# Kernel tuning notes

Hardware: AMD Instinct MI355X
Metric: run time of the kernel (lower is better)

Reference implementation:

```python
import jax, jax.numpy as jnp
import numpy as np
import math

H = 12
DH = 64
MAX_POS = 1024

def setup_inputs() -> dict:
    key = jax.random.key(0)
    ks = jax.random.split(key, 8)
    B, L, D = 2, 1024, 768
    s = 0.02
    return {
        "hidden_states": jax.random.normal(ks[0], (B, L, D), jnp.float32),
        "attention_mask": jnp.zeros((B, 1, 1, L), jnp.float32),
        "struct_matrix": jax.random.uniform(ks[1], (5, B, 1, L, L), jnp.float32),
        "Wq": jax.random.normal(ks[2], (D, D), jnp.float32) * s,
        "bq": jnp.zeros((D,), jnp.float32),
        "Wk": jax.random.normal(ks[3], (D, D), jnp.float32) * s,
        "bk": jnp.zeros((D,), jnp.float32),
        "Wv": jax.random.normal(ks[4], (D, D), jnp.float32) * s,
        "bv": jnp.zeros((D,), jnp.float32),
        "dist_emb": jax.random.normal(ks[5], (2 * MAX_POS - 1, DH), jnp.float32) * s,
        "ssan_w": jax.random.normal(ks[6], (5, H, DH, DH), jnp.float32) * s,
        "abs_bias": jnp.zeros((5, H), jnp.float32),
    }

def reference(hidden_states, attention_mask, struct_matrix, Wq, bq, Wk, bk, Wv, bv, dist_emb, ssan_w, abs_bias):
    B, L, D = hidden_states.shape

    def heads(x):  # [B,L,D] -> [B,H,L,dh]
        return x.reshape(B, L, H, DH).transpose(0, 2, 1, 3)

    q = heads(hidden_states @ Wq + bq)
    k = heads(hidden_states @ Wk + bk)
    v = heads(hidden_states @ Wv + bv)

    scores = jnp.einsum('bhqd,bhkd->bhqk', q, k)

    # relative_key_query positional scores
    pos_ids = jnp.arange(L)
    distance = pos_ids[:, None] - pos_ids[None, :]          # [L,L]
    pos = dist_emb[distance + MAX_POS - 1]                  # [L,L,dh]
    scores = scores + jnp.einsum('bhld,lrd->bhlr', q, pos)
    scores = scores + jnp.einsum('bhrd,lrd->bhlr', k, pos)

    scores = scores / math.sqrt(DH)
    scores = scores + attention_mask

    # 5 SSAN bilinear bias terms, masked by structural matrices
    for i in range(5):
        bias = jnp.einsum('bhqd,hde,bhke->bhqk', q, ssan_w[i], k)
        scores = scores + (bias + abs_bias[i][None, :, None, None]) * struct_matrix[i]

    probs = jax.nn.softmax(scores, axis=-1)
    ctx = jnp.einsum('bhqk,bhkd->bqhd', probs, v).reshape(B, L, D)
    return ctx
```

## Files before the change

### kernel.cpp

```cpp
#include <hip/hip_runtime.h>
#include <math.h>

#define NB 2
#define NL 1024
#define ND 768
#define NH 12
#define DH 64

typedef _Float16 f16;
typedef _Float16 f16x2 __attribute__((ext_vector_type(2)));
typedef _Float16 f16x4 __attribute__((ext_vector_type(4)));
typedef _Float16 f16x8 __attribute__((ext_vector_type(8)));
typedef float f32x4 __attribute__((ext_vector_type(4)));

#define MFMA16(a, b, c) __builtin_amdgcn_mfma_f32_16x16x32_f16((a), (b), (c), 0, 0, 0)

__device__ __forceinline__ void soft_barrier() {
    asm volatile("s_waitcnt lgkmcnt(0)\n\ts_barrier" ::: "memory");
}

__global__ __launch_bounds__(256) void prep_kernel(
    const float* __restrict__ hs,
    const float* __restrict__ Wq, const float* __restrict__ Wk,
    const float* __restrict__ Wv, const float* __restrict__ sw,
    const float* __restrict__ de,
    f16* __restrict__ hsf, f16* __restrict__ wt, f16* __restrict__ swt,
    f16* __restrict__ de16)
{
    __shared__ float sT[64 * 66];
    const int t = threadIdx.x;
    const int tile = blockIdx.x;

    if (tile < 768) {
        const int base = tile * 2048 + t * 8;
        float4 a = *(const float4*)&hs[base];
        float4 b = *(const float4*)&hs[base + 4];
        f16x8 hv;
        hv[0] = (f16)a.x; hv[1] = (f16)a.y; hv[2] = (f16)a.z; hv[3] = (f16)a.w;
        hv[4] = (f16)b.x; hv[5] = (f16)b.y; hv[6] = (f16)b.z; hv[7] = (f16)b.w;
        *(f16x8*)&hsf[base] = hv;
        return;
    }
    if (tile >= 1260) {
        const int base = (tile - 1260) * 2048 + t * 8;
        if (base < 2047 * 64) {
            float4 a = *(const float4*)&de[base];
            float4 b = *(const float4*)&de[base + 4];
            f16x8 hv;
            hv[0] = (f16)a.x; hv[1] = (f16)a.y; hv[2] = (f16)a.z; hv[3] = (f16)a.w;
            hv[4] = (f16)b.x; hv[5] = (f16)b.y; hv[6] = (f16)b.z; hv[7] = (f16)b.w;
            *(f16x8*)&de16[base] = hv;
        }
        return;
    }

    const float* S; f16* D; int sRS, dRS;
    const int ti = tile - 768;
    if (ti < 432) {
        const int mat = ti / 144, r2 = ti % 144, ht = r2 / 12, kt = r2 % 12;
        const float* W = (mat == 0) ? Wq : (mat == 1) ? Wk : Wv;
        S = W + (size_t)(kt * 64) * ND + ht * 64;
        D = wt + (size_t)((mat * NH + ht) * 64) * ND + kt * 64;
        sRS = ND; dRS = ND;
    } else {
        const int i = ti - 432;
        S = sw + (size_t)i * 4096;
        D = swt + (size_t)i * 4096;
        sRS = 64; dRS = 64;
    }

    {
        const int kk = t >> 2, nb = (t & 3) * 16;
        float v[16];
        #pragma unroll
        for (int j = 0; j < 4; ++j)
            *(float4*)&v[4 * j] = *(const float4*)&S[(size_t)kk * sRS + nb + 4 * j];
        #pragma unroll
        for (int jj = 0; jj < 16; ++jj)
            sT[(nb + jj) * 66 + kk] = v[jj];
    }
    soft_barrier();
    {
        const int n = t >> 2, kb = (t & 3) * 16;
        f16 tmp[16];
        #pragma unroll
        for (int j = 0; j < 8; ++j) {
            float2 x = *(float2*)&sT[n * 66 + kb + 2 * j];
            tmp[2 * j]     = (f16)x.x;
            tmp[2 * j + 1] = (f16)x.y;
        }
        *(f16x8*)&D[(size_t)n * dRS + kb]     = *(f16x8*)&tmp[0];
        *(f16x8*)&D[(size_t)n * dRS + kb + 8] = *(f16x8*)&tmp[8];
    }
}

__global__ __launch_bounds__(256, 2) void qkv_kernel(
    const f16* __restrict__ hsf, const f16* __restrict__ wt,
    const float* __restrict__ bq, const float* __restrict__ bk,
    const float* __restrict__ bv,
    f16* __restrict__ qf, f16* __restrict__ kf, f16* __restrict__ vt)
{
    __shared__ f16 sAB[2][2][128 * 72];

    const int m0 = blockIdx.x * 128;
    const int n0 = blockIdx.y * 128;
    const int mat = n0 / 768;
    const int h0  = (n0 % 768) / 64;
    const int bb  = m0 >> 10;
    const int l0  = m0 & 1023;

    const int t = threadIdx.x, lane = t & 63, w = t >> 6;
    const int quad = lane >> 4, l15 = lane & 15;
    const int wm = w >> 1, wn = w & 1;

    const float* bias = (mat == 0) ? bq : (mat == 1) ? bk : bv;

    const int srow = t >> 1;
    const int scol = (t & 1) * 32;
    const f16* Ag = hsf + (size_t)(m0 + srow) * ND + scol;
    const f16* Bg = wt  + (size_t)(n0 + srow) * ND + scol;

    f16x8 ar[4], br[4];
    f32x4 acc[4][4];
    #pragma unroll
    for (int mi = 0; mi < 4; ++mi)
        #pragma unroll
        for (int ni = 0; ni < 4; ++ni)
            acc[mi][ni] = (f32x4){0.f, 0.f, 0.f, 0.f};

    #pragma unroll
    for (int j = 0; j < 4; ++j) {
        ar[j] = *(const f16x8*)&Ag[8 * j];
        br[j] = *(const f16x8*)&Bg[8 * j];
    }
    #pragma unroll
    for (int j = 0; j < 4; ++j) {
        *(f16x8*)&sAB[0][0][srow * 72 + scol + 8 * j] = ar[j];
        *(f16x8*)&sAB[0][1][srow * 72 + scol + 8 * j] = br[j];
    }

    for (int kt2 = 0; kt2 < 12; ++kt2) {
        const int cur = kt2 & 1;
        soft_barrier();
        if (kt2 < 11) {
            const int k0 = (kt2 + 1) * 64;
            #pragma unroll
            for (int j = 0; j < 4; ++j) {
                ar[j] = *(const f16x8*)&Ag[k0 + 8 * j];
                br[j] = *(const f16x8*)&Bg[k0 + 8 * j];
            }
        }
        #pragma unroll
        for (int kk = 0; kk < 64; kk += 32) {
            const int ko = kk + quad * 8;
            f16x8 af[4], bf[4];
            #pragma unroll
            for (int i = 0; i < 4; ++i) {
                af[i] = *(f16x8*)&sAB[cur][0][(64 * wm + 16 * i + l15) * 72 + ko];
                bf[i] = *(f16x8*)&sAB[cur][1][(64 * wn + 16 * i + l15) * 72 + ko];
            }
            #pragma unroll
            for (int mi = 0; mi < 4; ++mi)
                #pragma unroll
                for (int ni = 0; ni < 4; ++ni)
                    acc[mi][ni] = MFMA16(af[mi], bf[ni], acc[mi][ni]);
        }
        if (kt2 < 11) {
            #pragma unroll
            for (int j = 0; j < 4; ++j) {
                *(f16x8*)&sAB[cur ^ 1][0][srow * 72 + scol + 8 * j] = ar[j];
                *(f16x8*)&sAB[cur ^ 1][1][srow * 72 + scol + 8 * j] = br[j];
            }
        }
    }
    soft_barrier();

    f16* sC = (f16*)sAB;
    float bz[4];
    #pragma unroll
    for (int ni = 0; ni < 4; ++ni)
        bz[ni] = bias[(n0 % 768) + 64 * wn + 16 * ni + l15];

    #pragma unroll
    for (int mi = 0; mi < 4; ++mi)
        #pragma unroll
        for (int ni = 0; ni < 4; ++ni) {
            const int col = 64 * wn + 16 * ni + l15;
            #pragma unroll
            for (int r = 0; r < 4; ++r) {
                const int row = 64 * wm + 16 * mi + 4 * quad + r;
                const f16 v = (f16)(acc[mi][ni][r] + bz[ni]);
                if (mat == 2) sC[col * 136 + row] = v;
                else          sC[row * 136 + col] = v;
            }
        }
    soft_barrier();

    if (mat < 2) {
        const int row = t >> 1, half = t & 1;
        f16* dst = ((mat == 0) ? qf : kf)
                 + ((size_t)(bb * NH + h0 + half) * NL + l0 + row) * DH;
        #pragma unroll
        for (int j = 0; j < 8; ++j)
            *(f16x8*)&dst[8 * j] = *(f16x8*)&sC[row * 136 + 64 * half + 8 * j];
    } else {
        const int c = t >> 1, half = t & 1;
        const int d = c & 63, hh = h0 + (c >> 6);
        f16* dst = vt + ((size_t)(bb * NH + hh) * DH + d) * NL + l0 + 64 * half;
        #pragma unroll
        for (int j = 0; j < 8; ++j)
            *(f16x8*)&dst[8 * j] = *(f16x8*)&sC[c * 136 + 64 * half + 8 * j];
    }
}

__global__ __launch_bounds__(256, 2) void attn_kernel(
    const f16* __restrict__ qf, const f16* __restrict__ kf,
    const f16* __restrict__ vt, const f16* __restrict__ swt,
    const float* __restrict__ mask, const float* __restrict__ struct_m,
    const f16* __restrict__ de16, const float* __restrict__ abs_bias,
    float* __restrict__ out)
{
    __shared__ f16 sK[64 * 72];
    __shared__ f16 sVt[2][64 * 72];
    __shared__ f16 sE[96 * 72];
    __shared__ f16 sQEl[96 * 34];
    __shared__ f16 sKEl[96 * 34];
    __shared__ float sS[32 * 68];
    __shared__ f16 sP[32 * 72];
    __shared__ float sAlpha[32], sL[32];

    const int l0 = blockIdx.x * 32;
    const int bh = blockIdx.y;
    const int bb = bh / NH, h = bh % NH;
    const int t  = threadIdx.x;
    const int lane  = t & 63;
    const int w     = t >> 6;
    const int quad  = lane >> 4;
    const int l15   = lane & 15;
    const int msub  = w >> 1;
    const int npair = w & 1;

    f16x8 aQ[2], aW[5][2];
    {
        const size_t qrow = ((size_t)bh * NL + l0 + 16 * msub + l15) * DH;
        #pragma unroll
        for (int K = 0; K < 2; ++K)
            aQ[K] = *(const f16x8*)&qf[qrow + 32 * K + 8 * quad];
    }

    {
        #pragma unroll
        for (int b = 0; b < 2; ++b) {
            const int pb0  = (b == 0) ? 0 : 3;
            const int pcnt = (b == 0) ? 3 : 2;
            #pragma unroll
            for (int pi = 0; pi < 3; ++pi) {
                if (pi < pcnt) {
                    const int p = pb0 + pi;
                    const f16* Wp = swt + ((size_t)(p * NH + h)) * 64 * 64;
                    #pragma unroll
                    for (int ntl = 0; ntl < 2; ++ntl) {
                        const int nt = 2 * npair + ntl;
                        f32x4 c = (f32x4){0.f, 0.f, 0.f, 0.f};
                        #pragma unroll
                        for (int K = 0; K < 2; ++K) {
                            f16x8 bw = *(const f16x8*)&Wp[(size_t)(16 * nt + l15) * 64 + 32 * K + 8 * quad];
                            c = MFMA16(aQ[K], bw, c);
                        }
                        #pragma unroll
                        for (int r = 0; r < 4; ++r)
                            sE[(pi * 32 + 16 * msub + 4 * quad + r) * 72 + 16 * nt + l15] = (f16)c[r];
                    }
                }
            }
            soft_barrier();
            #pragma unroll
            for (int pi = 0; pi < 3; ++pi) {
                if (pi < pcnt) {
                    #pragma unroll
                    for (int K = 0; K < 2; ++K)
                        aW[pb0 + pi][K] =
                            *(const f16x8*)&sE[(pi * 32 + 16 * msub + l15) * 72 + 32 * K + 8 * quad];
                }
            }
            soft_barrier();
        }
    }

    float ab[5];
    #pragma unroll
    for (int p = 0; p < 5; ++p) ab[p] = abs_bias[p * NH + h];

    float pf_st[5][2][4], pf_mask[2];
    f16x8 kreg[2], vreg[2], ereg[3];

    auto issue_kv = [&](int r0s) {
        const int row = t >> 3, col = (t & 7) * 8;
        const f16* ks = kf + ((size_t)bh * NL + r0s) * DH;
        kreg[0] = *(const f16x8*)&ks[row * 64 + col];
        kreg[1] = *(const f16x8*)&ks[(row + 32) * 64 + col];
        const f16* vs = vt + (size_t)bh * DH * NL + r0s;
        vreg[0] = *(const f16x8*)&vs[(size_t)row * NL + col];
        vreg[1] = *(const f16x8*)&vs[(size_t)(row + 32) * NL + col];
    };
    auto write_kv = [&](int buf) {
        const int row = t >> 3, col = (t & 7) * 8;
        *(f16x8*)&sK[row * 72 + col]             = kreg[0];
        *(f16x8*)&sK[(row + 32) * 72 + col]      = kreg[1];
        *(f16x8*)&sVt[buf][row * 72 + col]       = vreg[0];
        *(f16x8*)&sVt[buf][(row + 32) * 72 + col] = vreg[1];
    };
    auto issue_E = [&](int r0s) {
        const int ebase = l0 - r0s + 960;
        #pragma unroll
        for (int p2 = 0; p2 < 3; ++p2) {
            const int idx = t + 256 * p2;
            const int er = idx >> 3, colE = (idx & 7) * 8;
            if (er < 95)
                ereg[p2] = *(const f16x8*)&de16[(size_t)(ebase + er) * DH + colE];
        }
    };
    auto write_E = [&]() {
        #pragma unroll
        for (int p2 = 0; p2 < 3; ++p2) {
            const int idx = t + 256 * p2;
            const int er = idx >> 3, colE = (idx & 7) * 8;
            if (er < 95)
                *(f16x8*)&sE[er * 72 + colE] = ereg[p2];
        }
    };
    auto prefetch = [&](int r0s) {
        #pragma unroll
        for (int n = 0; n < 2; ++n) {
            const int j = 32 * npair + 16 * n + l15;
            pf_mask[n] = mask[bb * NL + r0s + j];
            #pragma unroll
            for (int r = 0; r < 4; ++r) {
                const int i = 16 * msub + 4 * quad + r;
                #pragma unroll
                for (int p = 0; p < 5; ++p)
                    pf_st[p][n][r] =
                        struct_m[((size_t)(p * NB + bb) * NL + l0 + i) * NL + r0s + j];
            }
        }
    };

    issue_kv(0);
    issue_E(0);
    write_kv(0);
    write_E();
    prefetch(0);

    const int sm_i = t >> 3;
    const int sm_jb = t & 7;
    float m_cur = -INFINITY, l_cur = 0.f;
    f32x4 O[2];
    O[0] = (f32x4){0.f, 0.f, 0.f, 0.f};
    O[1] = (f32x4){0.f, 0.f, 0.f, 0.f};

    soft_barrier();

    for (int kt = 0; kt < 16; ++kt) {
        const int cur = kt & 1;

        {
            const int krow = (16 * w + l15) * 72;
            f16x8 ak0 = *(f16x8*)&sK[krow + quad * 8];
            f16x8 ak1 = *(f16x8*)&sK[krow + 32 + quad * 8];
            #pragma unroll
            for (int c = 0; c < 3; ++c) {
                const int nt = 3 - w + c;
                const int erow = (16 * nt + l15) * 72;
                f16x8 e0 = *(f16x8*)&sE[erow + quad * 8];
                f16x8 e1 = *(f16x8*)&sE[erow + 32 + quad * 8];
                f32x4 ck = (f32x4){0.f, 0.f, 0.f, 0.f};
                ck = MFMA16(ak0, e0, ck);
                ck = MFMA16(ak1, e1, ck);
                const int base = (16 * nt + l15) * 34 + 16 * w + 4 * quad;
                f16x2 lo = {(f16)ck[0], (f16)ck[1]};
                f16x2 hi = {(f16)ck[2], (f16)ck[3]};
                *(f16x2*)&sKEl[base]     = lo;
                *(f16x2*)&sKEl[base + 2] = hi;
            }
            const int qs = 3 * npair + msub;
            const int qc = 3 - npair;
            #pragma unroll
            for (int c = 0; c < 3; ++c) {
                if (c < qc) {
                    const int nt = qs + c;
                    const int erow = (16 * nt + l15) * 72;
                    f16x8 e0 = *(f16x8*)&sE[erow + quad * 8];
                    f16x8 e1 = *(f16x8*)&sE[erow + 32 + quad * 8];
                    f32x4 cq = (f32x4){0.f, 0.f, 0.f, 0.f};
                    cq = MFMA16(aQ[0], e0, cq);
                    cq = MFMA16(aQ[1], e1, cq);
                    const int base = (16 * nt + l15) * 34 + 16 * msub + 4 * quad;
                    f16x2 lo = {(f16)cq[0], (f16)cq[1]};
                    f16x2 hi = {(f16)cq[2], (f16)cq[3]};
                    *(f16x2*)&sQEl[base]     = lo;
                    *(f16x2*)&sQEl[base + 2] = hi;
                }
            }
        }
        soft_barrier();

        {
            if (kt < 15) {
                issue_kv((kt + 1) * 64);
                issue_E((kt + 1) * 64);
            }

            f32x4 acc[2][6];
            #pragma unroll
            for (int n = 0; n < 2; ++n)
                #pragma unroll
                for (int p = 0; p < 6; ++p)
                    acc[n][p] = (f32x4){0.f, 0.f, 0.f, 0.f};

            #pragma unroll
            for (int K = 0; K < 2; ++K) {
                const int koff = K * 32 + quad * 8;
                f16x8 bk2[2];
                #pragma unroll
                for (int n = 0; n < 2; ++n)
                    bk2[n] = *(f16x8*)&sK[(32 * npair + 16 * n + l15) * 72 + koff];
                #pragma unroll
                for (int n = 0; n < 2; ++n)
                    acc[n][0] = MFMA16(aQ[K], bk2[n], acc[n][0]);
                #pragma unroll
                for (int p = 0; p < 5; ++p)
                    #pragma unroll
                    for (int n = 0; n < 2; ++n)
                        acc[n][1 + p] = MFMA16(aW[p][K], bk2[n], acc[n][1 + p]);
            }

            #pragma unroll
            for (int n = 0; n < 2; ++n) {
                const int j = 32 * npair + 16 * n + l15;
                #pragma unroll
                for (int r = 0; r < 4; ++r) {
                    const int i = 16 * msub + 4 * quad + r;
                    const int tp = i - j + 63;
                    float posv = (float)sQEl[tp * 34 + i] + (float)sKEl[tp * 34 + j];
                    float s = (acc[n][0][r] + posv) * 0.125f + pf_mask[n];
                    #pragma unroll
                    for (int p = 0; p < 5; ++p)
                        s += (acc[n][1 + p][r] + ab[p]) * pf_st[p][n][r];
                    sS[i * 68 + j] = s;
                }
            }
        }
        soft_barrier();

        {
            float sv[8];
            float smax = -INFINITY;
            #pragma unroll
            for (int k = 0; k < 8; ++k) {
                sv[k] = sS[sm_i * 68 + sm_jb + 8 * k];
                smax = fmaxf(smax, sv[k]);
            }
            #pragma unroll
            for (int off = 4; off > 0; off >>= 1)
                smax = fmaxf(smax, __shfl_xor(smax, off, 8));
            const float m_new = fmaxf(m_cur, smax);
            const float alpha = __expf(m_cur - m_new);
            float rsum = 0.f;
            #pragma unroll
            for (int k = 0; k < 8; ++k) {
                float p = __expf(sv[k] - m_new);
                sP[sm_i * 72 + sm_jb + 8 * k] = (f16)p;
                rsum += p;
            }
            #pragma unroll
            for (int off = 4; off > 0; off >>= 1)
                rsum += __shfl_xor(rsum, off, 8);
            l_cur = l_cur * alpha + rsum;
            m_cur = m_new;
            if (sm_jb == 0) { sAlpha[sm_i] = alpha; sL[sm_i] = l_cur; }

            if (kt < 15) {
                write_kv(cur ^ 1);
                write_E();
                prefetch((kt + 1) * 64);
            }
        }
        soft_barrier();

        {
            float a4[4];
            #pragma unroll
            for (int r = 0; r < 4; ++r) a4[r] = sAlpha[16 * msub + 4 * quad + r];
            #pragma unroll
            for (int n = 0; n < 2; ++n)
                #pragma unroll
                for (int r = 0; r < 4; ++r) O[n][r] *= a4[r];

            const int prow = (16 * msub + l15) * 72;
            #pragma unroll
            for (int K = 0; K < 2; ++K) {
                const int koff = K * 32 + quad * 8;
                f16x8 pfr = *(f16x8*)&sP[prow + koff];
                #pragma unroll
                for (int n = 0; n < 2; ++n) {
                    f16x8 vfr = *(f16x8*)&sVt[cur][(32 * npair + 16 * n + l15) * 72 + koff];
                    O[n] = MFMA16(pfr, vfr, O[n]);
                }
            }
        }
    }

    float linv[4];
    #pragma unroll
    for (int r = 0; r < 4; ++r) linv[r] = 1.0f / sL[16 * msub + 4 * quad + r];
    #pragma unroll
    for (int n = 0; n < 2; ++n) {
        const int dh = 32 * npair + 16 * n + l15;
        #pragma unroll
        for (int r = 0; r < 4; ++r) {
            const int i = 16 * msub + 4 * quad + r;
            out[((size_t)bb * NL + l0 + i) * ND + h * DH + dh] = O[n][r] * linv[r];
        }
    }
}

extern "C" void kernel_launch(void* const* d_in, const int* in_sizes, int n_in,
                              void* d_out, int out_size, void* d_ws, size_t ws_size,
                              hipStream_t stream) {
    const float* hs   = (const float*)d_in[0];
    const float* mask = (const float*)d_in[1];
    const float* stm  = (const float*)d_in[2];
    const float* Wq   = (const float*)d_in[3];
    const float* bq   = (const float*)d_in[4];
    const float* Wk   = (const float*)d_in[5];
    const float* bk   = (const float*)d_in[6];
    const float* Wv   = (const float*)d_in[7];
    const float* bv   = (const float*)d_in[8];
    const float* de   = (const float*)d_in[9];
    const float* sw   = (const float*)d_in[10];
    const float* abb  = (const float*)d_in[11];
    float* outp = (float*)d_out;

    const size_t NQKV = (size_t)NB * NH * NL * DH;
    char* ws = (char*)d_ws;
    f16* qf   = (f16*)ws;                 ws += NQKV * 2;
    f16* kf   = (f16*)ws;                 ws += NQKV * 2;
    f16* vtb  = (f16*)ws;                 ws += NQKV * 2;
    f16* hsf  = (f16*)ws;                 ws += NQKV * 2;
    f16* wt   = (f16*)ws;                 ws += (size_t)2304 * 768 * 2;
    f16* swt  = (f16*)ws;                 ws += (size_t)245760 * 2;
    f16* de16 = (f16*)ws;

    prep_kernel<<<1324, 256, 0, stream>>>(hs, Wq, Wk, Wv, sw, de,
                                          hsf, wt, swt, de16);
    qkv_kernel<<<dim3(16, 18), 256, 0, stream>>>(hsf, wt, bq, bk, bv, qf, kf, vtb);
    attn_kernel<<<dim3(32, 24), 256, 0, stream>>>(qf, kf, vtb, swt,
                                                  mask, stm, de16, abb, outp);
}
```

Measured before the change: 218.3 us.

## Swizzle shared memory layouts, halve QKV tile M, single-buffer V in attention

Replaces padded shared-memory rows (stride 72) with an XOR-swizzled 64-wide layout in both the QKV GEMM and the attention kernel, which shrinks LDS while still avoiding bank conflicts. The QKV GEMM tile shrinks from 128 to 64 rows, doubling the grid to improve CU occupancy and balance for this small problem. In attention, V is now single-buffered in LDS with register ping-pong prefetch, and the alpha/l scratch is folded into padding columns of the score buffer, cutting LDS footprint so more blocks can be resident. The risk is that writing V into the single buffer just before the PV product could add latency.

```diff
diff --git a/kernel.cpp b/kernel.cpp
--- a/kernel.cpp
+++ b/kernel.cpp
@@ -14,6 +14,8 @@
 typedef float f32x4 __attribute__((ext_vector_type(4)));
 
 #define MFMA16(a, b, c) __builtin_amdgcn_mfma_f32_16x16x32_f16((a), (b), (c), 0, 0, 0)
+
+#define SWZ(r, c) ((r) * 64 + ((c) ^ (((r) & 7) << 3)))
 
 __device__ __forceinline__ void soft_barrier() {
     asm volatile("s_waitcnt lgkmcnt(0)\n\ts_barrier" ::: "memory");
@@ -100,9 +102,10 @@
     const float* __restrict__ bv,
     f16* __restrict__ qf, f16* __restrict__ kf, f16* __restrict__ vt)
 {
-    __shared__ f16 sAB[2][2][128 * 72];
-
-    const int m0 = blockIdx.x * 128;
+    __shared__ f16 sA[2][64 * 64];
+    __shared__ f16 sB2[2][128 * 64];
+
+    const int m0 = blockIdx.x * 64;
     const int n0 = blockIdx.y * 128;
     const int mat = n0 / 768;
     const int h0  = (n0 % 768) / 64;
@@ -115,101 +118,101 @@
 
     const float* bias = (mat == 0) ? bq : (mat == 1) ? bk : bv;
 
-    const int srow = t >> 1;
-    const int scol = (t & 1) * 32;
-    const f16* Ag = hsf + (size_t)(m0 + srow) * ND + scol;
-    const f16* Bg = wt  + (size_t)(n0 + srow) * ND + scol;
-
-    f16x8 ar[4], br[4];
-    f32x4 acc[4][4];
-    #pragma unroll
-    for (int mi = 0; mi < 4; ++mi)
+    const int arow = t >> 2, acb = (t & 3) * 16;
+    const int brow = t >> 1, bcb = (t & 1) * 32;
+    const f16* Ag = hsf + (size_t)(m0 + arow) * ND + acb;
+    const f16* Bg = wt  + (size_t)(n0 + brow) * ND + bcb;
+
+    f16x8 ar[2], br[4];
+    f32x4 acc[2][4];
+    #pragma unroll
+    for (int mi = 0; mi < 2; ++mi)
         #pragma unroll
         for (int ni = 0; ni < 4; ++ni)
             acc[mi][ni] = (f32x4){0.f, 0.f, 0.f, 0.f};
 
-    #pragma unroll
-    for (int j = 0; j < 4; ++j) {
-        ar[j] = *(const f16x8*)&Ag[8 * j];
-        br[j] = *(const f16x8*)&Bg[8 * j];
-    }
-    #pragma unroll
-    for (int j = 0; j < 4; ++j) {
-        *(f16x8*)&sAB[0][0][srow * 72 + scol + 8 * j] = ar[j];
-        *(f16x8*)&sAB[0][1][srow * 72 + scol + 8 * j] = br[j];
-    }
+    ar[0] = *(const f16x8*)&Ag[0];
+    ar[1] = *(const f16x8*)&Ag[8];
+    #pragma unroll
+    for (int j = 0; j < 4; ++j) br[j] = *(const f16x8*)&Bg[8 * j];
+    *(f16x8*)&sA[0][SWZ(arow, acb)]     = ar[0];
+    *(f16x8*)&sA[0][SWZ(arow, acb + 8)] = ar[1];
+    #pragma unroll
+    for (int j = 0; j < 4; ++j)
+        *(f16x8*)&sB2[0][SWZ(brow, bcb + 8 * j)] = br[j];
 
     for (int kt2 = 0; kt2 < 12; ++kt2) {
         const int cur = kt2 & 1;
         soft_barrier();
         if (kt2 < 11) {
             const int k0 = (kt2 + 1) * 64;
-            #pragma unroll
-            for (int j = 0; j < 4; ++j) {
-                ar[j] = *(const f16x8*)&Ag[k0 + 8 * j];
-                br[j] = *(const f16x8*)&Bg[k0 + 8 * j];
-            }
+            ar[0] = *(const f16x8*)&Ag[k0];
+            ar[1] = *(const f16x8*)&Ag[k0 + 8];
+            #pragma unroll
+            for (int j = 0; j < 4; ++j) br[j] = *(const f16x8*)&Bg[k0 + 8 * j];
         }
         #pragma unroll
         for (int kk = 0; kk < 64; kk += 32) {
             const int ko = kk + quad * 8;
-            f16x8 af[4], bf[4];
-            #pragma unroll
-            for (int i = 0; i < 4; ++i) {
-                af[i] = *(f16x8*)&sAB[cur][0][(64 * wm + 16 * i + l15) * 72 + ko];
-                bf[i] = *(f16x8*)&sAB[cur][1][(64 * wn + 16 * i + l15) * 72 + ko];
-            }
-            #pragma unroll
-            for (int mi = 0; mi < 4; ++mi)
+            f16x8 af[2], bf[4];
+            #pragma unroll
+            for (int mi = 0; mi < 2; ++mi)
+                af[mi] = *(f16x8*)&sA[cur][SWZ(32 * wm + 16 * mi + l15, ko)];
+            #pragma unroll
+            for (int ni = 0; ni < 4; ++ni)
+                bf[ni] = *(f16x8*)&sB2[cur][SWZ(64 * wn + 16 * ni + l15, ko)];
+            #pragma unroll
+            for (int mi = 0; mi < 2; ++mi)
                 #pragma unroll
                 for (int ni = 0; ni < 4; ++ni)
                     acc[mi][ni] = MFMA16(af[mi], bf[ni], acc[mi][ni]);
         }
         if (kt2 < 11) {
-            #pragma unroll
-            for (int j = 0; j < 4; ++j) {
-                *(f16x8*)&sAB[cur ^ 1][0][srow * 72 + scol + 8 * j] = ar[j];
-                *(f16x8*)&sAB[cur ^ 1][1][srow * 72 + scol + 8 * j] = br[j];
-            }
+            *(f16x8*)&sA[cur ^ 1][SWZ(arow, acb)]     = ar[0];
+            *(f16x8*)&sA[cur ^ 1][SWZ(arow, acb + 8)] = ar[1];
+            #pragma unroll
+            for (int j = 0; j < 4; ++j)
+                *(f16x8*)&sB2[cur ^ 1][SWZ(brow, bcb + 8 * j)] = br[j];
         }
     }
     soft_barrier();
 
-    f16* sC = (f16*)sAB;
+    f16* sC = (f16*)sB2;
     float bz[4];
     #pragma unroll
     for (int ni = 0; ni < 4; ++ni)
         bz[ni] = bias[(n0 % 768) + 64 * wn + 16 * ni + l15];
 
     #pragma unroll
-    for (int mi = 0; mi < 4; ++mi)
+    for (int mi = 0; mi < 2; ++mi)
         #pragma unroll
         for (int ni = 0; ni < 4; ++ni) {
             const int col = 64 * wn + 16 * ni + l15;
             #pragma unroll
             for (int r = 0; r < 4; ++r) {
-                const int row = 64 * wm + 16 * mi + 4 * quad + r;
+                const int row = 32 * wm + 16 * mi + 4 * quad + r;
                 const f16 v = (f16)(acc[mi][ni][r] + bz[ni]);
-                if (mat == 2) sC[col * 136 + row] = v;
+                if (mat == 2) sC[col * 72 + row]  = v;
                 else          sC[row * 136 + col] = v;
             }
         }
     soft_barrier();
 
     if (mat < 2) {
-        const int row = t >> 1, half = t & 1;
+        const int r = t >> 2, q = t & 3;
+        const int col0 = 32 * q;
         f16* dst = ((mat == 0) ? qf : kf)
-                 + ((size_t)(bb * NH + h0 + half) * NL + l0 + row) * DH;
-        #pragma unroll
-        for (int j = 0; j < 8; ++j)
-            *(f16x8*)&dst[8 * j] = *(f16x8*)&sC[row * 136 + 64 * half + 8 * j];
+                 + ((size_t)(bb * NH + h0 + (q >> 1)) * NL + l0 + r) * DH + 32 * (q & 1);
+        #pragma unroll
+        for (int j = 0; j < 4; ++j)
+            *(f16x8*)&dst[8 * j] = *(f16x8*)&sC[r * 136 + col0 + 8 * j];
     } else {
         const int c = t >> 1, half = t & 1;
-        const int d = c & 63, hh = h0 + (c >> 6);
-        f16* dst = vt + ((size_t)(bb * NH + hh) * DH + d) * NL + l0 + 64 * half;
-        #pragma unroll
-        for (int j = 0; j < 8; ++j)
-            *(f16x8*)&dst[8 * j] = *(f16x8*)&sC[c * 136 + 64 * half + 8 * j];
+        f16* dst = vt + ((size_t)(bb * NH + h0 + (c >> 6)) * DH + (c & 63)) * NL
+                 + l0 + 32 * half;
+        #pragma unroll
+        for (int j = 0; j < 4; ++j)
+            *(f16x8*)&dst[8 * j] = *(f16x8*)&sC[c * 72 + 32 * half + 8 * j];
     }
 }
 
@@ -220,14 +223,13 @@
     const f16* __restrict__ de16, const float* __restrict__ abs_bias,
     float* __restrict__ out)
 {
-    __shared__ f16 sK[64 * 72];
-    __shared__ f16 sVt[2][64 * 72];
-    __shared__ f16 sE[96 * 72];
+    __shared__ f16 sK[64 * 64];
+    __shared__ f16 sVt[64 * 64];
+    __shared__ f16 sE[96 * 64];
     __shared__ f16 sQEl[96 * 34];
     __shared__ f16 sKEl[96 * 34];
-    __shared__ float sS[32 * 68];
-    __shared__ f16 sP[32 * 72];
-    __shared__ float sAlpha[32], sL[32];
+    __shared__ float sS[32 * 66];
+    __shared__ f16 sP[32 * 64];
 
     const int l0 = blockIdx.x * 32;
     const int bh = blockIdx.y;
@@ -269,7 +271,7 @@
                         }
                         #pragma unroll
                         for (int r = 0; r < 4; ++r)
-                            sE[(pi * 32 + 16 * msub + 4 * quad + r) * 72 + 16 * nt + l15] = (f16)c[r];
+                            sE[SWZ(pi * 32 + 16 * msub + 4 * quad + r, 16 * nt + l15)] = (f16)c[r];
                     }
                 }
             }
@@ -280,7 +282,7 @@
                     #pragma unroll
                     for (int K = 0; K < 2; ++K)
                         aW[pb0 + pi][K] =
-                            *(const f16x8*)&sE[(pi * 32 + 16 * msub + l15) * 72 + 32 * K + 8 * quad];
+                            *(const f16x8*)&sE[SWZ(pi * 32 + 16 * msub + l15, 32 * K + 8 * quad)];
                 }
             }
             soft_barrier();
@@ -292,23 +294,37 @@
     for (int p = 0; p < 5; ++p) ab[p] = abs_bias[p * NH + h];
 
     float pf_st[5][2][4], pf_mask[2];
-    f16x8 kreg[2], vreg[2], ereg[3];
-
-    auto issue_kv = [&](int r0s) {
-        const int row = t >> 3, col = (t & 7) * 8;
+    f16x8 kreg[2], ereg[3];
+    f16x8 vbufA[2], vbufB[2];
+
+    const int krow = t >> 3, kcol = (t & 7) * 8;
+
+    auto issue_k = [&](int r0s) {
         const f16* ks = kf + ((size_t)bh * NL + r0s) * DH;
-        kreg[0] = *(const f16x8*)&ks[row * 64 + col];
-        kreg[1] = *(const f16x8*)&ks[(row + 32) * 64 + col];
+        kreg[0] = *(const f16x8*)&ks[krow * 64 + kcol];
+        kreg[1] = *(const f16x8*)&ks[(krow + 32) * 64 + kcol];
+    };
+    auto write_k = [&]() {
+        *(f16x8*)&sK[SWZ(krow, kcol)]      = kreg[0];
+        *(f16x8*)&sK[SWZ(krow + 32, kcol)] = kreg[1];
+    };
+    auto issue_vA = [&](int r0s) {
         const f16* vs = vt + (size_t)bh * DH * NL + r0s;
-        vreg[0] = *(const f16x8*)&vs[(size_t)row * NL + col];
-        vreg[1] = *(const f16x8*)&vs[(size_t)(row + 32) * NL + col];
-    };
-    auto write_kv = [&](int buf) {
-        const int row = t >> 3, col = (t & 7) * 8;
-        *(f16x8*)&sK[row * 72 + col]             = kreg[0];
-        *(f16x8*)&sK[(row + 32) * 72 + col]      = kreg[1];
-        *(f16x8*)&sVt[buf][row * 72 + col]       = vreg[0];
-        *(f16x8*)&sVt[buf][(row + 32) * 72 + col] = vreg[1];
+        vbufA[0] = *(const f16x8*)&vs[(size_t)krow * NL + kcol];
+        vbufA[1] = *(const f16x8*)&vs[(size_t)(krow + 32) * NL + kcol];
+    };
+    auto issue_vB = [&](int r0s) {
+        const f16* vs = vt + (size_t)bh * DH * NL + r0s;
+        vbufB[0] = *(const f16x8*)&vs[(size_t)krow * NL + kcol];
+        vbufB[1] = *(const f16x8*)&vs[(size_t)(krow + 32) * NL + kcol];
+    };
+    auto write_vA = [&]() {
+        *(f16x8*)&sVt[SWZ(krow, kcol)]      = vbufA[0];
+        *(f16x8*)&sVt[SWZ(krow + 32, kcol)] = vbufA[1];
+    };
+    auto write_vB = [&]() {
+        *(f16x8*)&sVt[SWZ(krow, kcol)]      = vbufB[0];
+        *(f16x8*)&sVt[SWZ(krow + 32, kcol)] = vbufB[1];
     };
     auto issue_E = [&](int r0s) {
         const int ebase = l0 - r0s + 960;
@@ -326,7 +342,7 @@
             const int idx = t + 256 * p2;
             const int er = idx >> 3, colE = (idx & 7) * 8;
             if (er < 95)
-                *(f16x8*)&sE[er * 72 + colE] = ereg[p2];
+                *(f16x8*)&sE[SWZ(er, colE)] = ereg[p2];
         }
     };
     auto prefetch = [&](int r0s) {
@@ -345,11 +361,12 @@
         }
     };
 
-    issue_kv(0);
+    issue_k(0);
     issue_E(0);
-    write_kv(0);
+    issue_vA(0);
+    prefetch(0);
+    write_k();
     write_E();
-    prefetch(0);
 
     const int sm_i = t >> 3;
     const int sm_jb = t & 7;
@@ -361,18 +378,15 @@
     soft_barrier();
 
     for (int kt = 0; kt < 16; ++kt) {
-        const int cur = kt & 1;
 
         {
-            const int krow = (16 * w + l15) * 72;
-            f16x8 ak0 = *(f16x8*)&sK[krow + quad * 8];
-            f16x8 ak1 = *(f16x8*)&sK[krow + 32 + quad * 8];
+            f16x8 ak0 = *(f16x8*)&sK[SWZ(16 * w + l15, quad * 8)];
+            f16x8 ak1 = *(f16x8*)&sK[SWZ(16 * w + l15, 32 + quad * 8)];
             #pragma unroll
             for (int c = 0; c < 3; ++c) {
                 const int nt = 3 - w + c;
-                const int erow = (16 * nt + l15) * 72;
-                f16x8 e0 = *(f16x8*)&sE[erow + quad * 8];
-                f16x8 e1 = *(f16x8*)&sE[erow + 32 + quad * 8];
+                f16x8 e0 = *(f16x8*)&sE[SWZ(16 * nt + l15, quad * 8)];
+                f16x8 e1 = *(f16x8*)&sE[SWZ(16 * nt + l15, 32 + quad * 8)];
                 f32x4 ck = (f32x4){0.f, 0.f, 0.f, 0.f};
                 ck = MFMA16(ak0, e0, ck);
                 ck = MFMA16(ak1, e1, ck);
@@ -388,9 +402,8 @@
             for (int c = 0; c < 3; ++c) {
                 if (c < qc) {
                     const int nt = qs + c;
-                    const int erow = (16 * nt + l15) * 72;
-                    f16x8 e0 = *(f16x8*)&sE[erow + quad * 8];
-                    f16x8 e1 = *(f16x8*)&sE[erow + 32 + quad * 8];
+                    f16x8 e0 = *(f16x8*)&sE[SWZ(16 * nt + l15, quad * 8)];
+                    f16x8 e1 = *(f16x8*)&sE[SWZ(16 * nt + l15, 32 + quad * 8)];
                     f32x4 cq = (f32x4){0.f, 0.f, 0.f, 0.f};
                     cq = MFMA16(aQ[0], e0, cq);
                     cq = MFMA16(aQ[1], e1, cq);
@@ -405,8 +418,10 @@
         soft_barrier();
 
         {
+            if ((kt & 1) == 0) write_vA(); else write_vB();
             if (kt < 15) {
-                issue_kv((kt + 1) * 64);
+                issue_k((kt + 1) * 64);
+                if ((kt & 1) == 0) issue_vB((kt + 1) * 64); else issue_vA((kt + 1) * 64);
                 issue_E((kt + 1) * 64);
             }
 
@@ -423,7 +438,7 @@
                 f16x8 bk2[2];
                 #pragma unroll
                 for (int n = 0; n < 2; ++n)
-                    bk2[n] = *(f16x8*)&sK[(32 * npair + 16 * n + l15) * 72 + koff];
+                    bk2[n] = *(f16x8*)&sK[SWZ(32 * npair + 16 * n + l15, koff)];
                 #pragma unroll
                 for (int n = 0; n < 2; ++n)
                     acc[n][0] = MFMA16(aQ[K], bk2[n], acc[n][0]);
@@ -446,7 +461,7 @@
                     #pragma unroll
                     for (int p = 0; p < 5; ++p)
                         s += (acc[n][1 + p][r] + ab[p]) * pf_st[p][n][r];
-                    sS[i * 68 + j] = s;
+                    sS[i * 66 + j] = s;
                 }
             }
         }
@@ -457,7 +472,7 @@
             float smax = -INFINITY;
             #pragma unroll
             for (int k = 0; k < 8; ++k) {
-                sv[k] = sS[sm_i * 68 + sm_jb + 8 * k];
+                sv[k] = sS[sm_i * 66 + sm_jb + 8 * k];
                 smax = fmaxf(smax, sv[k]);
             }
             #pragma unroll
@@ -469,7 +484,7 @@
             #pragma unroll
             for (int k = 0; k < 8; ++k) {
                 float p = __expf(sv[k] - m_new);
-                sP[sm_i * 72 + sm_jb + 8 * k] = (f16)p;
+                sP[SWZ(sm_i, sm_jb + 8 * k)] = (f16)p;
                 rsum += p;
             }
             #pragma unroll
@@ -477,10 +492,13 @@
                 rsum += __shfl_xor(rsum, off, 8);
             l_cur = l_cur * alpha + rsum;
             m_cur = m_new;
-            if (sm_jb == 0) { sAlpha[sm_i] = alpha; sL[sm_i] = l_cur; }
+            if (sm_jb == 0) {
+                sS[sm_i * 66 + 64] = alpha;
+                sS[sm_i * 66 + 65] = l_cur;
+            }
 
             if (kt < 15) {
-                write_kv(cur ^ 1);
+                write_k();
                 write_E();
                 prefetch((kt + 1) * 64);
             }
@@ -490,20 +508,20 @@
         {
             float a4[4];
             #pragma unroll
-            for (int r = 0; r < 4; ++r) a4[r] = sAlpha[16 * msub + 4 * quad + r];
+            for (int r = 0; r < 4; ++r)
+                a4[r] = sS[(16 * msub + 4 * quad + r) * 66 + 64];
             #pragma unroll
             for (int n = 0; n < 2; ++n)
                 #pragma unroll
                 for (int r = 0; r < 4; ++r) O[n][r] *= a4[r];
 
-            const int prow = (16 * msub + l15) * 72;
             #pragma unroll
             for (int K = 0; K < 2; ++K) {
                 const int koff = K * 32 + quad * 8;
-                f16x8 pfr = *(f16x8*)&sP[prow + koff];
+                f16x8 pfr = *(f16x8*)&sP[SWZ(16 * msub + l15, koff)];
                 #pragma unroll
                 for (int n = 0; n < 2; ++n) {
-                    f16x8 vfr = *(f16x8*)&sVt[cur][(32 * npair + 16 * n + l15) * 72 + koff];
+                    f16x8 vfr = *(f16x8*)&sVt[SWZ(32 * npair + 16 * n + l15, koff)];
                     O[n] = MFMA16(pfr, vfr, O[n]);
                 }
             }
@@ -512,7 +530,8 @@
 
     float linv[4];
     #pragma unroll
-    for (int r = 0; r < 4; ++r) linv[r] = 1.0f / sL[16 * msub + 4 * quad + r];
+    for (int r = 0; r < 4; ++r)
+        linv[r] = 1.0f / sS[(16 * msub + 4 * quad + r) * 66 + 65];
     #pragma unroll
     for (int n = 0; n < 2; ++n) {
         const int dh = 32 * npair + 16 * n + l15;
@@ -553,7 +572,7 @@
 
     prep_kernel<<<1324, 256, 0, stream>>>(hs, Wq, Wk, Wv, sw, de,
                                           hsf, wt, swt, de16);
-    qkv_kernel<<<dim3(16, 18), 256, 0, stream>>>(hsf, wt, bq, bk, bv, qf, kf, vtb);
+    qkv_kernel<<<dim3(32, 18), 256, 0, stream>>>(hsf, wt, bq, bk, bv, qf, kf, vtb);
     attn_kernel<<<dim3(32, 24), 256, 0, stream>>>(qf, kf, vtb, swt,
                                                   mask, stm, de16, abb, outp);
 }
```

Measured after the change: 255.0 us. 1.17x slower.
